# Performance work log

Measured on AMD Instinct MI355X. Metric: run time of the kernel, lower is better.

The kernel has to match this reference:

```python
import jax, jax.numpy as jnp
import numpy as np

N, D, P = 4096, 1024, 2048
TAU, ALPHA = 0.2, 0.8
GAMMA_EX, GAMMA_IN = 2.0, 1.6
EPS = 1e-8


def _cos_sim(e):
    # F.cosine_similarity(e[:,None], e[None,:], dim=2) == normalized rows matmul
    n = jnp.linalg.norm(e, axis=1, keepdims=True)
    en = e / jnp.maximum(n, EPS)
    return en @ en.T  # [N, N]


def setup_inputs() -> dict:
    key = jax.random.key(0)
    embeddings = jax.random.normal(key, (N, D), dtype=jnp.float32)
    # positive pairs: (0,1),(2,3),... (arange fill)
    pp = np.arange(2 * P).reshape(P, 2)
    pos_partner = np.arange(N)
    pos_partner[pp[:, 0]] = pp[:, 1]
    pos_partner[pp[:, 1]] = pp[:, 0]
    # negative pairs = all ordered (i,j), i!=j, minus ordered positive tuples,
    # enumerated row-major (deterministic stand-in for torch's set order).
    pos_m = np.zeros((N, N), dtype=bool)
    pos_m[pp[:, 0], pp[:, 1]] = True
    neg_m = ~np.eye(N, dtype=bool) & ~pos_m
    ii, jj = np.nonzero(neg_m)  # row-major order
    neg_partner = np.arange(N)
    neg_partner[ii] = jj
    neg_partner[jj] = ii  # processed[j] = ... overwrites after
    return {
        "embeddings": embeddings,
        "positive_pairs": jnp.asarray(pp, jnp.int32),
        "pos_partner": jnp.asarray(pos_partner, jnp.int32),
        "neg_partner": jnp.asarray(neg_partner, jnp.int32),
    }


def reference(embeddings, positive_pairs, pos_partner, neg_partner):
    pi, pj = positive_pairs[:, 0], positive_pairs[:, 1]
    # Beta(gamma,gamma) scalar mixing coefficients (dim_mixing=False)
    lam_pos = jax.random.beta(jax.random.key(1), GAMMA_EX, GAMMA_EX) + 1.0  # 'ex'
    lam_neg = jax.random.beta(jax.random.key(2), GAMMA_IN, GAMMA_IN)        # 'in'

    orig = _cos_sim(embeddings)
    hp = _cos_sim(lam_pos * embeddings + (1.0 - lam_pos) * embeddings[pos_partner])
    hn = _cos_sim(lam_neg * embeddings + (1.0 - lam_neg) * embeddings[neg_partner])

    eye = jnp.eye(N, dtype=bool)
    pos_m = jnp.zeros((N, N), dtype=bool).at[pi, pj].set(True)  # ordered positives
    neg_m = ~eye & ~pos_m                                        # ordered negatives
    # pos replacement first, then neg replacement overwrites (faithful ordering)
    sim = jnp.where(pos_m | pos_m.T, hp, orig)
    sim = jnp.where(neg_m | neg_m.T, hn, sim)

    # ----- compute_loss (stage='train': quantile hard-negative mining) -----
    mask = eye | pos_m | pos_m.T
    exp_sim = jnp.exp(sim / TAU)
    exp_masked = jnp.where(mask, 0.0, exp_sim)
    pos_ij = exp_sim[pi, pj]
    pos_ji = exp_sim[pj, pi]
    exp_i = exp_masked[pi]  # [P, N]
    exp_j = exp_masked[pj]
    thr_i = jnp.quantile(exp_i, ALPHA, axis=1, keepdims=True)
    thr_j = jnp.quantile(exp_j, ALPHA, axis=1, keepdims=True)
    sum_i = jnp.where(exp_i >= thr_i, exp_i, 0.0).sum(axis=1)
    sum_j = jnp.where(exp_j >= thr_j, exp_j, 0.0).sum(axis=1)
    loss_ij = -jnp.log(pos_ij / (pos_ij + sum_i))
    loss_ji = -jnp.log(pos_ji / (pos_ji + sum_j))
    return (loss_ij + loss_ji).sum() / (2 * P)
```

## Files before the change

kernel.cpp:

```cpp
#include <hip/hip_runtime.h>
#include <hip/hip_bf16.h>

#define NN 4096
#define DD 1024
constexpr float LAM = 0.45f;
constexpr float INV_TAU = 5.0f;
constexpr int KSEL = 820;
constexpr unsigned KEY_BASE = 0x3B80u;
constexpr int NBINS = 2048;

typedef __attribute__((ext_vector_type(8))) short bf16x8;
typedef __attribute__((ext_vector_type(4))) float f32x4;

__device__ inline void async_copy16(const ushort* g, ushort* l) {
    __builtin_amdgcn_global_load_lds(
        (const __attribute__((address_space(1))) void*)g,
        (__attribute__((address_space(3))) void*)l, 16, 0, 0);
}

__global__ __launch_bounds__(256) void mixnorm_kernel(const float* __restrict__ E,
                                                      const int* __restrict__ negp,
                                                      ushort* __restrict__ U) {
    int r = blockIdx.x, t = threadIdx.x;
    int p = negp[r];
    const float a = LAM, b = 1.0f - LAM;
    float4 x = ((const float4*)(E + (size_t)r * DD))[t];
    float4 y = ((const float4*)(E + (size_t)p * DD))[t];
    float4 m;
    m.x = a * x.x + b * y.x;
    m.y = a * x.y + b * y.y;
    m.z = a * x.z + b * y.z;
    m.w = a * x.w + b * y.w;
    float ss = m.x * m.x + m.y * m.y + m.z * m.z + m.w * m.w;
    #pragma unroll
    for (int off = 32; off > 0; off >>= 1) ss += __shfl_down(ss, off, 64);
    __shared__ float part[4];
    if ((t & 63) == 0) part[t >> 6] = ss;
    __syncthreads();
    float tot = part[0] + part[1] + part[2] + part[3];
    float inv = 1.0f / fmaxf(sqrtf(tot), 1e-8f);
    ushort4 o;
    o.x = __bfloat16_as_ushort(__float2bfloat16(m.x * inv));
    o.y = __bfloat16_as_ushort(__float2bfloat16(m.y * inv));
    o.z = __bfloat16_as_ushort(__float2bfloat16(m.z * inv));
    o.w = __bfloat16_as_ushort(__float2bfloat16(m.w * inv));
    ((ushort4*)(U + (size_t)r * DD))[t] = o;
}

__global__ __launch_bounds__(512) void gemm_exp_kernel(const ushort* __restrict__ U,
                                                       ushort* __restrict__ Z) {
    __shared__ ushort sm_all[16384];
    ushort* A = sm_all;
    ushort* B = sm_all + 8192;
    const int t = threadIdx.x;
    const int w = t >> 6, l = t & 63;

    const int m = blockIdx.x;
    float fdec = sqrtf(8.0f * (float)m + 1.0f);
    int by = (int)((fdec - 1.0f) * 0.5f);
    while ((by + 1) * (by + 2) / 2 <= m) by++;
    while (by * (by + 1) / 2 > m) by--;
    const int bx = m - by * (by + 1) / 2;

    const ushort* gA = U + (size_t)(by * 128 + (t >> 2)) * DD + (t & 3) * 8;
    const ushort* gB = U + (size_t)(bx * 128 + (t >> 2)) * DD + (t & 3) * 8;
    ushort* lA0 = A + w * 512;
    ushort* lA1 = A + 4096 + w * 512;
    ushort* lB0 = B + w * 512;
    ushort* lB1 = B + 4096 + w * 512;

    f32x4 acc[2][4];
    #pragma unroll
    for (int i = 0; i < 2; i++)
        #pragma unroll
        for (int j = 0; j < 4; j++) acc[i][j] = (f32x4){0.f, 0.f, 0.f, 0.f};

    const int wr = w >> 1, wc = w & 1;
    const int mrow = wr * 32 + (l & 15);
    const int nrow = wc * 64 + (l & 15);
    const int kq = (l >> 4) * 8;

    for (int k0 = 0; k0 < DD; k0 += 64) {
        async_copy16(gA, lA0);
        async_copy16(gA + 32, lA1);
        async_copy16(gB, lB0);
        async_copy16(gB + 32, lB1);
        gA += 64; gB += 64;
        __syncthreads();
        #pragma unroll
        for (int kh = 0; kh < 2; kh++) {
            const ushort* Ah = A + kh * 4096;
            const ushort* Bh = B + kh * 4096;
            bf16x8 af[2], bfr[4];
            #pragma unroll
            for (int i = 0; i < 2; i++)
                af[i] = *(const bf16x8*)(Ah + (mrow + i * 16) * 32 + kq);
            #pragma unroll
            for (int j = 0; j < 4; j++)
                bfr[j] = *(const bf16x8*)(Bh + (nrow + j * 16) * 32 + kq);
            #pragma unroll
            for (int i = 0; i < 2; i++)
                #pragma unroll
                for (int j = 0; j < 4; j++)
                    acc[i][j] = __builtin_amdgcn_mfma_f32_16x16x32_bf16(af[i], bfr[j], acc[i][j], 0, 0, 0);
        }
        __syncthreads();
    }

    ushort* smv = sm_all;
    ushort* smT = sm_all + 4096;
    const bool mirror = (bx != by);
    #pragma unroll
    for (int h = 0; h < 4; h++) {
        __syncthreads();
        if (wr == h) {
            #pragma unroll
            for (int i = 0; i < 2; i++)
                #pragma unroll
                for (int j = 0; j < 4; j++)
                    #pragma unroll
                    for (int rg = 0; rg < 4; rg++) {
                        float v = __expf(acc[i][j][rg] * INV_TAU);
                        ushort hv = __bfloat16_as_ushort(__float2bfloat16(v));
                        int lrow = i * 16 + ((l >> 4) << 2) + rg;
                        int lcol = (wc << 6) + j * 16 + (l & 15);
                        smv[lrow * 128 + lcol] = hv;
                        smT[lcol * 48 + lrow] = hv;
                    }
        }
        __syncthreads();
        {
            const uint4* src = (const uint4*)(smv + (t >> 4) * 128 + (t & 15) * 8);
            uint4* dst = (uint4*)(Z + (size_t)(by * 128 + h * 32 + (t >> 4)) * NN + bx * 128 + (t & 15) * 8);
            *dst = *src;
        }
        if (mirror) {
            const uint4* srcT = (const uint4*)(smT + (t >> 2) * 48 + (t & 3) * 8);
            uint4* dstT = (uint4*)(Z + (size_t)(bx * 128 + (t >> 2)) * NN + by * 128 + h * 32 + (t & 3) * 8);
            *dstT = *srcT;
        }
    }
}

__global__ __launch_bounds__(256) void rowloss_kernel(const ushort* __restrict__ Z,
                                                      const int* __restrict__ posp,
                                                      float* __restrict__ loss) {
    const int t = threadIdx.x, w = t >> 6, l = t & 63;
    const int r = blockIdx.x * 4 + w;
    const int p = posp[r];
    const uint4* zr = (const uint4*)(Z + (size_t)r * NN);

    const float posv = __uint_as_float(((unsigned)Z[(size_t)r * NN + p]) << 16);

    unsigned ko[32];
    #pragma unroll
    for (int c = 0; c < 8; c++) {
        uint4 v = zr[c * 64 + l];
        unsigned wd[4] = {v.x, v.y, v.z, v.w};
        const int cb = (c * 64 + l) * 8;
        #pragma unroll
        for (int q = 0; q < 4; q++) {
            int c0 = cb + 2 * q, c1 = c0 + 1;
            unsigned x = wd[q];
            unsigned klo = (c0 == p || c0 == r) ? 0u : (x & 0xFFFFu);
            unsigned khi = (c1 == p || c1 == r) ? 0u : (x >> 16);
            ko[c * 4 + q] = klo | (khi << 16) | 0x80008000u;
        }
    }

    unsigned lo_b = KEY_BASE, hi_b = KEY_BASE + NBINS;
    #pragma unroll 1
    for (int it = 0; it < 11; it++) {
        unsigned mid = (lo_b + hi_b) >> 1;
        unsigned mm = mid | (mid << 16);
        unsigned a = 0;
        #pragma unroll
        for (int i = 0; i < 32; i++)
            a += ((ko[i] - mm) >> 15) & 0x10001u;
        #pragma unroll
        for (int d = 1; d < 64; d <<= 1) a += __shfl_xor(a, d, 64);
        unsigned c = (a & 0xFFFFu) + (a >> 16);
        bool ge = (c >= (unsigned)KSEL);
        lo_b = ge ? mid : lo_b;
        hi_b = ge ? hi_b : mid;
    }
    const unsigned thr = lo_b;

    float s0 = 0.f, s1 = 0.f;
    #pragma unroll
    for (int i = 0; i < 32; i++) {
        unsigned x = ko[i] & 0x7FFF7FFFu;
        unsigned klo = x & 0xFFFFu;
        unsigned khi = x >> 16;
        float vlo = __uint_as_float(klo << 16);
        float vhi = __uint_as_float(x & 0xFFFF0000u);
        s0 += (klo >= thr) ? vlo : 0.f;
        s1 += (khi >= thr) ? vhi : 0.f;
    }
    float s = s0 + s1;
    #pragma unroll
    for (int d = 1; d < 64; d <<= 1) s += __shfl_xor(s, d, 64);
    if (l == 0) loss[r] = log1pf(s / posv);
}

__global__ __launch_bounds__(256) void finalize_kernel(const float* __restrict__ loss,
                                                       unsigned* __restrict__ out) {
    __shared__ float part[4];
    const int t = threadIdx.x, w = t >> 6, l = t & 63;
    float s = 0.f;
    #pragma unroll
    for (int q = 0; q < 4; q++) {
        float4 v = ((const float4*)loss)[t * 4 + q];
        s += (v.x + v.y) + (v.z + v.w);
    }
    #pragma unroll
    for (int off = 32; off > 0; off >>= 1) s += __shfl_down(s, off, 64);
    if (l == 0) part[w] = s;
    __syncthreads();
    if (t == 0) {
        float v = (part[0] + part[1] + part[2] + part[3]) * (1.0f / 4096.0f);
        unsigned short bits = __bfloat16_as_ushort(__float2bfloat16(v));
        *out = ((unsigned)bits << 16) | (unsigned)bits;
    }
}

extern "C" void kernel_launch(void* const* d_in, const int* in_sizes, int n_in,
                              void* d_out, int out_size, void* d_ws, size_t ws_size,
                              hipStream_t stream) {
    const float* E = (const float*)d_in[0];
    const int* posp = (const int*)d_in[2];
    const int* negp = (const int*)d_in[3];

    float* loss = (float*)d_ws;
    ushort* U = (ushort*)((char*)d_ws + 16384);
    ushort* Z = (ushort*)((char*)d_ws + 16384 + (size_t)NN * DD * 2);

    mixnorm_kernel<<<NN, 256, 0, stream>>>(E, negp, U);
    gemm_exp_kernel<<<528, 512, 0, stream>>>(U, Z);
    rowloss_kernel<<<NN / 4, 256, 0, stream>>>(Z, posp, loss);
    finalize_kernel<<<1, 256, 0, stream>>>(loss, (unsigned*)d_out);
}
```

Baseline: 123.1 us.

## Halve GEMM block to 256 threads with 64x64 per-warp tiles

The symmetric GEMM+exp kernel now runs 4 waves per block instead of 8. Each wave computes a 64x64 output sub-tile (4x4 MFMA fragments) rather than 32x64. Loads and the epilogue stores are looped so fewer threads cover the same 128x128 tile. This raises register-level reuse of A/B fragments per LDS read and cuts synchronisation overhead, at the cost of more accumulator registers and fewer waves to hide latency.

```diff
diff --git a/kernel.cpp b/kernel.cpp
--- a/kernel.cpp
+++ b/kernel.cpp
@@ -47,7 +47,7 @@
     ((ushort4*)(U + (size_t)r * DD))[t] = o;
 }
 
-__global__ __launch_bounds__(512) void gemm_exp_kernel(const ushort* __restrict__ U,
+__global__ __launch_bounds__(256) void gemm_exp_kernel(const ushort* __restrict__ U,
                                                        ushort* __restrict__ Z) {
     __shared__ ushort sm_all[16384];
     ushort* A = sm_all;
@@ -64,42 +64,42 @@
 
     const ushort* gA = U + (size_t)(by * 128 + (t >> 2)) * DD + (t & 3) * 8;
     const ushort* gB = U + (size_t)(bx * 128 + (t >> 2)) * DD + (t & 3) * 8;
-    ushort* lA0 = A + w * 512;
-    ushort* lA1 = A + 4096 + w * 512;
-    ushort* lB0 = B + w * 512;
-    ushort* lB1 = B + 4096 + w * 512;
-
-    f32x4 acc[2][4];
-    #pragma unroll
-    for (int i = 0; i < 2; i++)
+    const size_t rstep = (size_t)64 * DD;
+
+    f32x4 acc[4][4];
+    #pragma unroll
+    for (int i = 0; i < 4; i++)
         #pragma unroll
         for (int j = 0; j < 4; j++) acc[i][j] = (f32x4){0.f, 0.f, 0.f, 0.f};
 
     const int wr = w >> 1, wc = w & 1;
-    const int mrow = wr * 32 + (l & 15);
+    const int mrow = wr * 64 + (l & 15);
     const int nrow = wc * 64 + (l & 15);
     const int kq = (l >> 4) * 8;
 
     for (int k0 = 0; k0 < DD; k0 += 64) {
-        async_copy16(gA, lA0);
-        async_copy16(gA + 32, lA1);
-        async_copy16(gB, lB0);
-        async_copy16(gB + 32, lB1);
+        #pragma unroll
+        for (int kh = 0; kh < 2; kh++) {
+            async_copy16(gA + kh * 32,         A + kh * 4096 + w * 512);
+            async_copy16(gA + rstep + kh * 32, A + kh * 4096 + 2048 + w * 512);
+            async_copy16(gB + kh * 32,         B + kh * 4096 + w * 512);
+            async_copy16(gB + rstep + kh * 32, B + kh * 4096 + 2048 + w * 512);
+        }
         gA += 64; gB += 64;
         __syncthreads();
         #pragma unroll
         for (int kh = 0; kh < 2; kh++) {
             const ushort* Ah = A + kh * 4096;
             const ushort* Bh = B + kh * 4096;
-            bf16x8 af[2], bfr[4];
-            #pragma unroll
-            for (int i = 0; i < 2; i++)
+            bf16x8 af[4], bfr[4];
+            #pragma unroll
+            for (int i = 0; i < 4; i++)
                 af[i] = *(const bf16x8*)(Ah + (mrow + i * 16) * 32 + kq);
             #pragma unroll
             for (int j = 0; j < 4; j++)
                 bfr[j] = *(const bf16x8*)(Bh + (nrow + j * 16) * 32 + kq);
             #pragma unroll
-            for (int i = 0; i < 2; i++)
+            for (int i = 0; i < 4; i++)
                 #pragma unroll
                 for (int j = 0; j < 4; j++)
                     acc[i][j] = __builtin_amdgcn_mfma_f32_16x16x32_bf16(af[i], bfr[j], acc[i][j], 0, 0, 0);
@@ -113,16 +113,16 @@
     #pragma unroll
     for (int h = 0; h < 4; h++) {
         __syncthreads();
-        if (wr == h) {
-            #pragma unroll
-            for (int i = 0; i < 2; i++)
+        if (wr == (h >> 1)) {
+            #pragma unroll
+            for (int i2 = 0; i2 < 2; i2++)
                 #pragma unroll
                 for (int j = 0; j < 4; j++)
                     #pragma unroll
                     for (int rg = 0; rg < 4; rg++) {
-                        float v = __expf(acc[i][j][rg] * INV_TAU);
+                        float v = __expf(acc[(h & 1) * 2 + i2][j][rg] * INV_TAU);
                         ushort hv = __bfloat16_as_ushort(__float2bfloat16(v));
-                        int lrow = i * 16 + ((l >> 4) << 2) + rg;
+                        int lrow = i2 * 16 + ((l >> 4) << 2) + rg;
                         int lcol = (wc << 6) + j * 16 + (l & 15);
                         smv[lrow * 128 + lcol] = hv;
                         smT[lcol * 48 + lrow] = hv;
@@ -130,14 +130,26 @@
         }
         __syncthreads();
         {
-            const uint4* src = (const uint4*)(smv + (t >> 4) * 128 + (t & 15) * 8);
-            uint4* dst = (uint4*)(Z + (size_t)(by * 128 + h * 32 + (t >> 4)) * NN + bx * 128 + (t & 15) * 8);
-            *dst = *src;
+            #pragma unroll
+            for (int c = 0; c < 2; c++) {
+                int idx = c * 256 + t;
+                int row = idx >> 4;
+                int col8 = idx & 15;
+                const uint4* src = (const uint4*)(smv + row * 128 + col8 * 8);
+                uint4* dst = (uint4*)(Z + (size_t)(by * 128 + h * 32 + row) * NN + bx * 128 + col8 * 8);
+                *dst = *src;
+            }
         }
         if (mirror) {
-            const uint4* srcT = (const uint4*)(smT + (t >> 2) * 48 + (t & 3) * 8);
-            uint4* dstT = (uint4*)(Z + (size_t)(bx * 128 + (t >> 2)) * NN + by * 128 + h * 32 + (t & 3) * 8);
-            *dstT = *srcT;
+            #pragma unroll
+            for (int c = 0; c < 2; c++) {
+                int idx = c * 256 + t;
+                int row = idx >> 2;
+                int col8 = idx & 3;
+                const uint4* srcT = (const uint4*)(smT + row * 48 + col8 * 8);
+                uint4* dstT = (uint4*)(Z + (size_t)(bx * 128 + row) * NN + by * 128 + h * 32 + col8 * 8);
+                *dstT = *srcT;
+            }
         }
     }
 }
@@ -236,7 +248,7 @@
     ushort* Z = (ushort*)((char*)d_ws + 16384 + (size_t)NN * DD * 2);
 
     mixnorm_kernel<<<NN, 256, 0, stream>>>(E, negp, U);
-    gemm_exp_kernel<<<528, 512, 0, stream>>>(U, Z);
+    gemm_exp_kernel<<<528, 256, 0, stream>>>(U, Z);
     rowloss_kernel<<<NN / 4, 256, 0, stream>>>(Z, posp, loss);
     finalize_kernel<<<1, 256, 0, stream>>>(loss, (unsigned*)d_out);
 }
```

Result: slower. 132.0 us (+7.3%).

## Double-buffer GEMM LDS tiles with async prefetch and XOR-swizzled layout

Applied to the files above, without the earlier changes.

The GEMM main loop now uses two LDS buffers, issuing the next k-tile's global-to-LDS async copies before computing on the current tile, with explicit vmcnt waits and raw barriers replacing __syncthreads. The source column group is XOR-swizzled by row so that fragment reads from LDS hit different banks. This aims to hide global load latency behind MFMA work and cut LDS bank conflicts, at the cost of doubling shared memory to 64KB, which may lower occupancy.

```diff
diff --git a/kernel.cpp b/kernel.cpp
--- a/kernel.cpp
+++ b/kernel.cpp
@@ -49,9 +49,7 @@
 
 __global__ __launch_bounds__(512) void gemm_exp_kernel(const ushort* __restrict__ U,
                                                        ushort* __restrict__ Z) {
-    __shared__ ushort sm_all[16384];
-    ushort* A = sm_all;
-    ushort* B = sm_all + 8192;
+    __shared__ ushort sm_all[32768];
     const int t = threadIdx.x;
     const int w = t >> 6, l = t & 63;
 
@@ -62,12 +60,9 @@
     while (by * (by + 1) / 2 > m) by--;
     const int bx = m - by * (by + 1) / 2;
 
-    const ushort* gA = U + (size_t)(by * 128 + (t >> 2)) * DD + (t & 3) * 8;
-    const ushort* gB = U + (size_t)(bx * 128 + (t >> 2)) * DD + (t & 3) * 8;
-    ushort* lA0 = A + w * 512;
-    ushort* lA1 = A + 4096 + w * 512;
-    ushort* lB0 = B + w * 512;
-    ushort* lB1 = B + 4096 + w * 512;
+    const int cg = (t & 3) ^ ((t >> 3) & 3);
+    const ushort* gA = U + (size_t)(by * 128 + (t >> 2)) * DD + cg * 8;
+    const ushort* gB = U + (size_t)(bx * 128 + (t >> 2)) * DD + cg * 8;
 
     f32x4 acc[2][4];
     #pragma unroll
@@ -78,33 +73,54 @@
     const int wr = w >> 1, wc = w & 1;
     const int mrow = wr * 32 + (l & 15);
     const int nrow = wc * 64 + (l & 15);
-    const int kq = (l >> 4) * 8;
-
-    for (int k0 = 0; k0 < DD; k0 += 64) {
-        async_copy16(gA, lA0);
-        async_copy16(gA + 32, lA1);
-        async_copy16(gB, lB0);
-        async_copy16(gB + 32, lB1);
-        gA += 64; gB += 64;
-        __syncthreads();
+    const int kqs = ((l >> 4) ^ (((l & 15) >> 1) & 3)) * 8;
+
+    {
+        ushort* base = sm_all;
+        async_copy16(gA,      base + w * 512);
+        async_copy16(gA + 32, base + 4096 + w * 512);
+        async_copy16(gB,      base + 8192 + w * 512);
+        async_copy16(gB + 32, base + 12288 + w * 512);
+    }
+
+    int cur = 0;
+    for (int kt = 0; kt < 16; kt++) {
+        if (kt < 15) {
+            const ushort* ga = gA + (kt + 1) * 64;
+            const ushort* gb = gB + (kt + 1) * 64;
+            ushort* base = sm_all + (cur ^ 1) * 16384;
+            async_copy16(ga,      base + w * 512);
+            async_copy16(ga + 32, base + 4096 + w * 512);
+            async_copy16(gb,      base + 8192 + w * 512);
+            async_copy16(gb + 32, base + 12288 + w * 512);
+            asm volatile("s_waitcnt vmcnt(4)" ::: "memory");
+        } else {
+            asm volatile("s_waitcnt vmcnt(0)" ::: "memory");
+        }
+        __builtin_amdgcn_s_barrier();
+        asm volatile("" ::: "memory");
+        const ushort* Abase = sm_all + cur * 16384;
+        const ushort* Bbase = Abase + 8192;
         #pragma unroll
         for (int kh = 0; kh < 2; kh++) {
-            const ushort* Ah = A + kh * 4096;
-            const ushort* Bh = B + kh * 4096;
+            const ushort* Ah = Abase + kh * 4096;
+            const ushort* Bh = Bbase + kh * 4096;
             bf16x8 af[2], bfr[4];
             #pragma unroll
             for (int i = 0; i < 2; i++)
-                af[i] = *(const bf16x8*)(Ah + (mrow + i * 16) * 32 + kq);
+                af[i] = *(const bf16x8*)(Ah + (mrow + i * 16) * 32 + kqs);
             #pragma unroll
             for (int j = 0; j < 4; j++)
-                bfr[j] = *(const bf16x8*)(Bh + (nrow + j * 16) * 32 + kq);
+                bfr[j] = *(const bf16x8*)(Bh + (nrow + j * 16) * 32 + kqs);
             #pragma unroll
             for (int i = 0; i < 2; i++)
                 #pragma unroll
                 for (int j = 0; j < 4; j++)
                     acc[i][j] = __builtin_amdgcn_mfma_f32_16x16x32_bf16(af[i], bfr[j], acc[i][j], 0, 0, 0);
         }
-        __syncthreads();
+        asm volatile("" ::: "memory");
+        __builtin_amdgcn_s_barrier();
+        cur ^= 1;
     }
 
     ushort* smv = sm_all;
```

After: 124.1 us. Within noise of the previous version (+0.8%).

## Rewrite similarity GEMM with 256x256 tiles and triple-buffered async loads

Applied to the files above, without the earlier changes.

The exp-similarity GEMM no longer exploits symmetry with 528 triangular 128x128 tiles plus mirrored transpose stores. It now computes the full matrix with 256 blocks of 256x256 tiles, one per CU, mapped through an XCD-aware block swizzle. K-slices are triple-buffered in LDS via async global-to-LDS copies and explicit vmcnt waits. LDS addresses are XOR-swizzled to avoid bank conflicts, and MFMA phases run with raised wave priority. This should raise MFMA utilisation and cut per-block overhead, at the cost of doing twice the multiply work of the triangular scheme and carrying heavier register pressure from the 8x4 accumulators.

```diff
diff --git a/kernel.cpp b/kernel.cpp
--- a/kernel.cpp
+++ b/kernel.cpp
@@ -17,6 +17,9 @@
         (const __attribute__((address_space(1))) void*)g,
         (__attribute__((address_space(3))) void*)l, 16, 0, 0);
 }
+
+#define BAR() do { asm volatile("" ::: "memory"); __builtin_amdgcn_s_barrier(); \
+                   asm volatile("" ::: "memory"); } while (0)
 
 __global__ __launch_bounds__(256) void mixnorm_kernel(const float* __restrict__ E,
                                                       const int* __restrict__ negp,
@@ -47,97 +50,114 @@
     ((ushort4*)(U + (size_t)r * DD))[t] = o;
 }
 
-__global__ __launch_bounds__(512) void gemm_exp_kernel(const ushort* __restrict__ U,
-                                                       ushort* __restrict__ Z) {
-    __shared__ ushort sm_all[16384];
-    ushort* A = sm_all;
-    ushort* B = sm_all + 8192;
+__global__ __launch_bounds__(512, 2) void gemm_exp_kernel(const ushort* __restrict__ U,
+                                                          ushort* __restrict__ Z) {
+    __shared__ ushort sm[49152];
     const int t = threadIdx.x;
     const int w = t >> 6, l = t & 63;
-
-    const int m = blockIdx.x;
-    float fdec = sqrtf(8.0f * (float)m + 1.0f);
-    int by = (int)((fdec - 1.0f) * 0.5f);
-    while ((by + 1) * (by + 2) / 2 <= m) by++;
-    while (by * (by + 1) / 2 > m) by--;
-    const int bx = m - by * (by + 1) / 2;
-
-    const ushort* gA = U + (size_t)(by * 128 + (t >> 2)) * DD + (t & 3) * 8;
-    const ushort* gB = U + (size_t)(bx * 128 + (t >> 2)) * DD + (t & 3) * 8;
-    ushort* lA0 = A + w * 512;
-    ushort* lA1 = A + 4096 + w * 512;
-    ushort* lB0 = B + w * 512;
-    ushort* lB1 = B + 4096 + w * 512;
-
-    f32x4 acc[2][4];
-    #pragma unroll
-    for (int i = 0; i < 2; i++)
+    const int wr = w >> 2, wc = w & 3;
+
+    const int bid = blockIdx.x;
+    const int swz = (bid & 7) * 32 + (bid >> 3);
+    const int by = swz >> 4, bx = swz & 15;
+
+    const int srow = t >> 2;
+    const int scs = (t & 3) ^ (srow & 3);
+    const size_t sgo = (size_t)srow * DD + scs * 8;
+    const ushort* gA = U + (size_t)(by * 256) * DD;
+    const ushort* gB = U + (size_t)(bx * 256) * DD;
+    #define STAGEH(dst_u, gX, h, k2) \
+        async_copy16(gX + (size_t)(h) * 128 * DD + sgo + (k2), sm + (dst_u) + t * 8)
+
+    const int rA = l & 15;
+    const int sA8 = (((l >> 4) ^ (l & 3))) * 8;
+    const int brow = (wc & 1) * 64 + rA;
+    const int bh = (wc >> 1) * 4096;
+
+    f32x4 acc[8][4];
+    #pragma unroll
+    for (int i = 0; i < 8; i++)
         #pragma unroll
         for (int j = 0; j < 4; j++) acc[i][j] = (f32x4){0.f, 0.f, 0.f, 0.f};
 
-    const int wr = w >> 1, wc = w & 1;
-    const int mrow = wr * 32 + (l & 15);
-    const int nrow = wc * 64 + (l & 15);
-    const int kq = (l >> 4) * 8;
-
-    for (int k0 = 0; k0 < DD; k0 += 64) {
-        async_copy16(gA, lA0);
-        async_copy16(gA + 32, lA1);
-        async_copy16(gB, lB0);
-        async_copy16(gB + 32, lB1);
-        gA += 64; gB += 64;
-        __syncthreads();
-        #pragma unroll
-        for (int kh = 0; kh < 2; kh++) {
-            const ushort* Ah = A + kh * 4096;
-            const ushort* Bh = B + kh * 4096;
-            bf16x8 af[2], bfr[4];
-            #pragma unroll
-            for (int i = 0; i < 2; i++)
-                af[i] = *(const bf16x8*)(Ah + (mrow + i * 16) * 32 + kq);
+    STAGEH(0,             gA, 0, 0);   STAGEH(4096,          gA, 1, 0);
+    STAGEH(8192,          gB, 0, 0);   STAGEH(12288,         gB, 1, 0);
+    STAGEH(16384 + 0,     gA, 0, 32);  STAGEH(16384 + 4096,  gA, 1, 32);
+    STAGEH(16384 + 8192,  gB, 0, 32);  STAGEH(16384 + 12288, gB, 1, 32);
+
+    int bb = 0, tb = 2;
+    for (int kt = 0; kt < 32; kt++) {
+        const int k2 = (kt + 2) * 32;
+        const ushort* Ab = sm + bb * 16384 + wr * 4096;
+        const ushort* Bb = sm + bb * 16384 + 8192 + bh;
+        ushort* tbu = (ushort*)0;
+        const bool st = (kt <= 29);
+        const int tbase = tb * 16384;
+
+        if (kt == 31) asm volatile("s_waitcnt vmcnt(0)" ::: "memory");
+        else          asm volatile("s_waitcnt vmcnt(4)" ::: "memory");
+        if (st) { STAGEH(tbase, gA, 0, k2); STAGEH(tbase + 4096, gA, 1, k2); }
+        BAR();
+        {
+            bf16x8 bfr[4], af[4];
             #pragma unroll
             for (int j = 0; j < 4; j++)
-                bfr[j] = *(const bf16x8*)(Bh + (nrow + j * 16) * 32 + kq);
-            #pragma unroll
-            for (int i = 0; i < 2; i++)
+                bfr[j] = *(const bf16x8*)(Bb + (brow + j * 16) * 32 + sA8);
+            #pragma unroll
+            for (int i = 0; i < 4; i++)
+                af[i] = *(const bf16x8*)(Ab + (rA + i * 16) * 32 + sA8);
+            __builtin_amdgcn_s_setprio(1);
+            #pragma unroll
+            for (int i = 0; i < 4; i++)
                 #pragma unroll
                 for (int j = 0; j < 4; j++)
                     acc[i][j] = __builtin_amdgcn_mfma_f32_16x16x32_bf16(af[i], bfr[j], acc[i][j], 0, 0, 0);
-        }
-        __syncthreads();
-    }
-
-    ushort* smv = sm_all;
-    ushort* smT = sm_all + 4096;
-    const bool mirror = (bx != by);
-    #pragma unroll
-    for (int h = 0; h < 4; h++) {
-        __syncthreads();
-        if (wr == h) {
-            #pragma unroll
-            for (int i = 0; i < 2; i++)
+            __builtin_amdgcn_s_setprio(0);
+            BAR();
+
+            #pragma unroll
+            for (int i = 0; i < 4; i++)
+                af[i] = *(const bf16x8*)(Ab + (rA + (4 + i) * 16) * 32 + sA8);
+            if (st) { STAGEH(tbase + 8192, gB, 0, k2); STAGEH(tbase + 12288, gB, 1, k2); }
+            BAR();
+            __builtin_amdgcn_s_setprio(1);
+            #pragma unroll
+            for (int i = 0; i < 4; i++)
                 #pragma unroll
                 for (int j = 0; j < 4; j++)
-                    #pragma unroll
-                    for (int rg = 0; rg < 4; rg++) {
-                        float v = __expf(acc[i][j][rg] * INV_TAU);
-                        ushort hv = __bfloat16_as_ushort(__float2bfloat16(v));
-                        int lrow = i * 16 + ((l >> 4) << 2) + rg;
-                        int lcol = (wc << 6) + j * 16 + (l & 15);
-                        smv[lrow * 128 + lcol] = hv;
-                        smT[lcol * 48 + lrow] = hv;
-                    }
+                    acc[4 + i][j] = __builtin_amdgcn_mfma_f32_16x16x32_bf16(af[i], bfr[j], acc[4 + i][j], 0, 0, 0);
+            __builtin_amdgcn_s_setprio(0);
+            BAR();
         }
+        (void)tbu;
+        bb = (bb == 2) ? 0 : bb + 1;
+        tb = (tb == 2) ? 0 : tb + 1;
+    }
+    #undef STAGEH
+
+    #pragma unroll
+    for (int i = 0; i < 8; i++) {
         __syncthreads();
-        {
-            const uint4* src = (const uint4*)(smv + (t >> 4) * 128 + (t & 15) * 8);
-            uint4* dst = (uint4*)(Z + (size_t)(by * 128 + h * 32 + (t >> 4)) * NN + bx * 128 + (t & 15) * 8);
+        #pragma unroll
+        for (int j = 0; j < 4; j++)
+            #pragma unroll
+            for (int rg = 0; rg < 4; rg++) {
+                float v = __expf(acc[i][j][rg] * INV_TAU);
+                ushort hv = __bfloat16_as_ushort(__float2bfloat16(v));
+                int lrow = wr * 16 + ((l >> 4) << 2) + rg;
+                int lcol = wc * 64 + j * 16 + rA;
+                sm[lrow * 256 + lcol] = hv;
+            }
+        __syncthreads();
+        #pragma unroll
+        for (int q = 0; q < 2; q++) {
+            int n = q * 512 + t;
+            int row = n >> 5;
+            int c = n & 31;
+            int grow = by * 256 + (row >> 4) * 128 + i * 16 + (row & 15);
+            const uint4* src = (const uint4*)(sm + row * 256 + c * 8);
+            uint4* dst = (uint4*)(Z + (size_t)grow * NN + bx * 256 + c * 8);
             *dst = *src;
-        }
-        if (mirror) {
-            const uint4* srcT = (const uint4*)(smT + (t >> 2) * 48 + (t & 3) * 8);
-            uint4* dstT = (uint4*)(Z + (size_t)(bx * 128 + (t >> 2)) * NN + by * 128 + h * 32 + (t & 3) * 8);
-            *dstT = *srcT;
         }
     }
 }
@@ -236,7 +256,7 @@
     ushort* Z = (ushort*)((char*)d_ws + 16384 + (size_t)NN * DD * 2);
 
     mixnorm_kernel<<<NN, 256, 0, stream>>>(E, negp, U);
-    gemm_exp_kernel<<<528, 512, 0, stream>>>(U, Z);
+    gemm_exp_kernel<<<256, 512, 0, stream>>>(U, Z);
     rowloss_kernel<<<NN / 4, 256, 0, stream>>>(Z, posp, loss);
     finalize_kernel<<<1, 256, 0, stream>>>(loss, (unsigned*)d_out);
 }
```

Result: slower. 127.3 us (+3.5%).
